# Kernel tuning notes

Hardware: AMD Instinct MI355X
Metric: run time of the kernel (lower is better)

## Reference

```python
import jax, jax.numpy as jnp
import numpy as np

T_NUM = 1024      # tracks
DET_NUM = 1024    # detections
DEG = 64          # candidate detections per track
E = T_NUM * DEG   # directed track->det edges (row<col half)
N = T_NUM + DET_NUM
D_IN = 512
D_EMB = 256
LAM = 5.0
SLACK = -0.2
SINKHORN_ITERS = 8


def setup_inputs() -> dict:
    key = jax.random.key(0)
    ks = jax.random.split(key, 20)
    x = jax.random.normal(ks[0], (N, D_IN), jnp.float32)
    coords = jax.random.uniform(ks[1], (N, 4), dtype=jnp.float32)
    r = jax.random.uniform(ks[2], (N, 4), dtype=jnp.float32)
    bx1 = r[:, 0] * 100.0; by1 = r[:, 1] * 100.0
    bw = r[:, 2] * 50.0 + 1.0; bh = r[:, 3] * 50.0 + 1.0
    coords_original = jnp.stack([bx1, by1, bx1 + bw, by1 + bh], axis=1)
    src_t = jnp.repeat(jnp.arange(T_NUM, dtype=jnp.int32), DEG)
    off = jnp.tile(jnp.arange(DEG, dtype=jnp.int32), T_NUM)
    dst_d = (src_t * 13 + off) % DET_NUM            # unique det per (track, slot)
    src = src_t
    dst = dst_d + T_NUM                              # detection node ids come after tracks
    edge_index = jnp.concatenate([jnp.stack([src, dst]), jnp.stack([dst, src])], axis=1)
    ground_truth = jax.random.bernoulli(ks[3], 0.1, (T_NUM * DET_NUM,)).astype(jnp.float32)

    def lin(k, i, o):
        return jax.random.normal(k, (i, o), jnp.float32) / np.sqrt(i).astype(np.float32)

    params = {
        'W_enc': lin(ks[4], D_IN, D_EMB), 'b_enc': jnp.zeros((D_EMB,), jnp.float32),
        'W1a': lin(ks[5], 2 * D_EMB, 64), 'b1a': jnp.zeros((64,), jnp.float32),
        'W2a': lin(ks[6], 64, 1), 'b2a': jnp.zeros((1,), jnp.float32),
        'W1g': lin(ks[7], 8, 16), 'b1g': jnp.zeros((16,), jnp.float32),
        'W2g': lin(ks[8], 16, 1), 'b2g': jnp.zeros((1,), jnp.float32),
        'W1f': lin(ks[9], 2, 8), 'b1f': jnp.zeros((8,), jnp.float32),
        'W2f': lin(ks[10], 8, 1), 'b2f': jnp.zeros((1,), jnp.float32),
        'Wn': lin(ks[11], D_EMB, D_EMB), 'Wm': lin(ks[12], D_EMB, D_EMB),
        'bo': jnp.zeros((D_EMB,), jnp.float32),
        'W1c': lin(ks[13], 2, 8), 'b1c': jnp.zeros((8,), jnp.float32),
        'W2c': lin(ks[14], 8, 1), 'b2c': jnp.zeros((1,), jnp.float32),
    }
    out = {'x': x, 'coords': coords, 'coords_original': coords_original,
           'ground_truth': ground_truth, 'edge_index': edge_index}
    out.update(params)
    return out


def _box_iou(a, b):
    # a, b: [E, 4] boxes (x1, y1, x2, y2)
    lt = jnp.maximum(a[:, :2], b[:, :2])
    rb = jnp.minimum(a[:, 2:], b[:, 2:])
    wh = jnp.clip(rb - lt, 0.0)
    inter = wh[:, 0] * wh[:, 1]
    area_a = (a[:, 2] - a[:, 0]) * (a[:, 3] - a[:, 1])
    area_b = (b[:, 2] - b[:, 0]) * (b[:, 3] - b[:, 1])
    return inter / (area_a + area_b - inter + 1e-9)


def _sinkhorn(M):
    def body(M, _):
        M = M / (jnp.sum(M, axis=1, keepdims=True) + 1e-9)
        M = M / (jnp.sum(M, axis=0, keepdims=True) + 1e-9)
        return M, None
    M, _ = jax.lax.scan(body, M, None, length=SINKHORN_ITERS)
    return M


def _forward(x, coords, coords_original,
             W_enc, b_enc, W1a, b1a, W2a, b2a, W1g, b1g, W2g, b2g,
             W1f, b1f, W2f, b2f, Wn, Wm, bo, W1c, b1c, W2c, b2c,
             edge_index):
    node = jax.nn.relu(x @ W_enc + b_enc)                      # [N, D_EMB]
    src, dst = edge_index[0], edge_index[1]                    # [2E]
    # batched per-edge appearance affinity (replaces python edge loop)
    pair = jnp.concatenate([node[src], node[dst]], axis=1)     # [2E, 2*D_EMB]
    a1 = jax.nn.relu(pair @ W1a + b1a) @ W2a + b2a             # [2E, 1]
    geo = jnp.concatenate([coords[src], coords[dst]], axis=1)  # [2E, 8]
    a2 = jax.nn.relu(geo @ W1g + b1g) @ W2g + b2g              # [2E, 1]
    e_in = jnp.concatenate([a1, a2], axis=1)                   # [2E, 2]
    edge_emb = jax.nn.relu(e_in @ W1f + b1f) @ W2f + b2f       # [2E, 1]
    # optim_net: one round of edge-weighted message passing
    msg = jax.ops.segment_sum(edge_emb * node[src], dst, num_segments=N)
    out = jax.nn.relu(node @ Wn + msg @ Wm + bo)               # [N, D_EMB]
    # forward (row < col) edges are the first E entries by construction
    sf, df = src[:E], dst[:E]
    oa, ob = out[sf], out[df]
    denom = jnp.maximum(jnp.linalg.norm(oa, axis=1) * jnp.linalg.norm(ob, axis=1), 1e-6)
    cosv = jnp.sum(oa * ob, axis=1) / denom                    # CosineSimilarity(dim=0) per edge
    iou = _box_iou(coords_original[sf], coords_original[df])   # [E]
    f_in = jnp.stack([cosv, iou], axis=1)                      # [E, 2]
    aff = (jax.nn.relu(f_in @ W1c + b1c) @ W2c + b2c)[:, 0]    # [E]
    # assignment matrix with slack row/col, scatter exp(aff*lam)
    slack_val = jnp.exp(jnp.float32(SLACK * LAM))
    M = jnp.full((T_NUM + 1, DET_NUM + 1), slack_val, jnp.float32)
    M = M.at[:T_NUM, :DET_NUM].set(0.0)
    M = M.at[sf, df - T_NUM].set(jnp.exp(aff * LAM))
    M = _sinkhorn(M)
    return M[:-1, :-1].reshape(-1)                             # [T_NUM*DET_NUM]


def reference(x, coords, coords_original, ground_truth, edge_index,
              W_enc, b_enc, W1a, b1a, W2a, b2a, W1g, b1g, W2g, b2g,
              W1f, b1f, W2f, b2f, Wn, Wm, bo, W1c, b1c, W2c, b2c):
    normalized_output = _forward(x, coords, coords_original,
                                 W_enc, b_enc, W1a, b1a, W2a, b2a,
                                 W1g, b1g, W2g, b2g, W1f, b1f, W2f, b2f,
                                 Wn, Wm, bo, W1c, b1c, W2c, b2c, edge_index)
    det_num = jnp.asarray(DET_NUM, jnp.int32)
    tracklet_num = jnp.asarray(T_NUM, jnp.int32)
    return (normalized_output, ground_truth, det_num, tracklet_num)
```

## Files before the change

kernel.cpp:

```cpp
#include <hip/hip_runtime.h>

#define T_NUM 1024
#define DET_NUM 1024
#define E_NUM 65536
#define TWO_E 131072
#define N_NODES 2048
#define D_IN 512
#define D_EMB 256

__device__ __forceinline__ unsigned bf16r(float x) {
  const unsigned u = __float_as_uint(x);
  return (u + 0x7fffu + ((u >> 16) & 1u)) >> 16;
}
__device__ __forceinline__ float bflo(unsigned p) { return __uint_as_float(p << 16); }
__device__ __forceinline__ float bfhi(unsigned p) { return __uint_as_float(p & 0xffff0000u); }

__global__ __launch_bounds__(512) void k_enc_pg(
    const float* __restrict__ x, const float* __restrict__ W,
    const float* __restrict__ b, const float* __restrict__ coords,
    const float* __restrict__ W1a, const float* __restrict__ W1g,
    float* __restrict__ node, float* __restrict__ P1, float* __restrict__ P2,
    float* __restrict__ G1, float* __restrict__ G2) {
  __shared__ __align__(16) float ns[8][D_EMB];
  __shared__ __align__(16) float ps[8][D_EMB];
  const int tid = threadIdx.x;
  const int j = tid & 255;
  const int h = __builtin_amdgcn_readfirstlane(tid >> 8);
  const int row0 = blockIdx.x * 8;
  float acc[8];
  const float bj = b[j];
#pragma unroll
  for (int r = 0; r < 8; r++) acc[r] = (h == 0) ? bj : 0.f;
  const float* xr = x + (size_t)row0 * D_IN + h * 256;
  const float* Wp = W + (size_t)h * 256 * D_EMB;
  for (int k = 0; k < 256; k += 4) {
    const float w0 = Wp[(k + 0) * D_EMB + j];
    const float w1 = Wp[(k + 1) * D_EMB + j];
    const float w2 = Wp[(k + 2) * D_EMB + j];
    const float w3 = Wp[(k + 3) * D_EMB + j];
#pragma unroll
    for (int r = 0; r < 8; r++) {
      const float4 xv = *reinterpret_cast<const float4*>(xr + (size_t)r * D_IN + k);
      acc[r] = fmaf(xv.x, w0, acc[r]);
      acc[r] = fmaf(xv.y, w1, acc[r]);
      acc[r] = fmaf(xv.z, w2, acc[r]);
      acc[r] = fmaf(xv.w, w3, acc[r]);
    }
  }
  if (h == 1) {
#pragma unroll
    for (int r = 0; r < 8; r++) ps[r][j] = acc[r];
  }
  __syncthreads();
  if (h == 0) {
#pragma unroll
    for (int r = 0; r < 8; r++) {
      const float v = fmaxf(acc[r] + ps[r][j], 0.f);
      node[(size_t)(row0 + r) * D_EMB + j] = v;
      ns[r][j] = v;
    }
  }
  __syncthreads();
  {
    const int r = tid >> 6, hh = tid & 63;
    float a1 = 0.f, a2 = 0.f;
    for (int k = 0; k < D_EMB; k += 4) {
      const float4 nv = *reinterpret_cast<const float4*>(&ns[r][k]);
      a1 = fmaf(nv.x, W1a[(k + 0) * 64 + hh], a1);
      a1 = fmaf(nv.y, W1a[(k + 1) * 64 + hh], a1);
      a1 = fmaf(nv.z, W1a[(k + 2) * 64 + hh], a1);
      a1 = fmaf(nv.w, W1a[(k + 3) * 64 + hh], a1);
      a2 = fmaf(nv.x, W1a[(D_EMB + k + 0) * 64 + hh], a2);
      a2 = fmaf(nv.y, W1a[(D_EMB + k + 1) * 64 + hh], a2);
      a2 = fmaf(nv.z, W1a[(D_EMB + k + 2) * 64 + hh], a2);
      a2 = fmaf(nv.w, W1a[(D_EMB + k + 3) * 64 + hh], a2);
    }
    P1[(size_t)(row0 + r) * 64 + hh] = a1;
    P2[(size_t)(row0 + r) * 64 + hh] = a2;
  }
  if (tid < 128) {
    const int r = tid >> 4, hh = tid & 15;
    const int n = row0 + r;
    float g1 = 0.f, g2 = 0.f;
#pragma unroll
    for (int k = 0; k < 4; k++) {
      const float c = coords[(size_t)n * 4 + k];
      g1 = fmaf(c, W1g[k * 16 + hh], g1);
      g2 = fmaf(c, W1g[(4 + k) * 16 + hh], g2);
    }
    G1[(size_t)n * 16 + hh] = g1;
    G2[(size_t)n * 16 + hh] = g2;
  }
}

__global__ __launch_bounds__(256) void k_edge(
    const float* __restrict__ P1, const float* __restrict__ P2,
    const float* __restrict__ G1, const float* __restrict__ G2,
    const float* __restrict__ b1a, const float* __restrict__ W2a, const float* __restrict__ b2a,
    const float* __restrict__ b1g, const float* __restrict__ W2g, const float* __restrict__ b2g,
    const float* __restrict__ W1f, const float* __restrict__ b1f,
    const float* __restrict__ W2f, const float* __restrict__ b2f,
    float* __restrict__ wE) {
  const int e = blockIdx.x * 256 + threadIdx.x;
  int s, dn;
  if (e < E_NUM) {
    const int t = e >> 6, o = e & 63;
    s = t; dn = T_NUM + ((13 * t + o) & 1023);
  } else {
    const int e2 = e - E_NUM;
    const int t = e2 >> 6, o = e2 & 63;
    s = T_NUM + ((13 * t + o) & 1023); dn = t;
  }
  const float4* p1 = (const float4*)(P1 + (size_t)s * 64);
  const float4* p2 = (const float4*)(P2 + (size_t)dn * 64);
  const float4* b1 = (const float4*)b1a;
  const float4* w2 = (const float4*)W2a;
  float a1 = b2a[0];
#pragma unroll
  for (int i = 0; i < 16; i++) {
    const float4 pa = p1[i], pb = p2[i], bb = b1[i], ww = w2[i];
    a1 += fmaxf(pa.x + pb.x + bb.x, 0.f) * ww.x + fmaxf(pa.y + pb.y + bb.y, 0.f) * ww.y +
          fmaxf(pa.z + pb.z + bb.z, 0.f) * ww.z + fmaxf(pa.w + pb.w + bb.w, 0.f) * ww.w;
  }
  const float4* g1 = (const float4*)(G1 + (size_t)s * 16);
  const float4* g2 = (const float4*)(G2 + (size_t)dn * 16);
  const float4* bg = (const float4*)b1g;
  const float4* wg = (const float4*)W2g;
  float a2 = b2g[0];
#pragma unroll
  for (int i = 0; i < 4; i++) {
    const float4 pa = g1[i], pb = g2[i], bb = bg[i], ww = wg[i];
    a2 += fmaxf(pa.x + pb.x + bb.x, 0.f) * ww.x + fmaxf(pa.y + pb.y + bb.y, 0.f) * ww.y +
          fmaxf(pa.z + pb.z + bb.z, 0.f) * ww.z + fmaxf(pa.w + pb.w + bb.w, 0.f) * ww.w;
  }
  float acc = b2f[0];
#pragma unroll
  for (int jj = 0; jj < 8; jj++) {
    const float h = fmaxf(a1 * W1f[jj] + a2 * W1f[8 + jj] + b1f[jj], 0.f);
    acc = fmaf(h, W2f[jj], acc);
  }
  wE[e] = acc;
}

__global__ __launch_bounds__(256) void k_msg_out(
    const float* __restrict__ wE, const float* __restrict__ node,
    const float* __restrict__ Wn, const float* __restrict__ Wm,
    const float* __restrict__ bo, float* __restrict__ outE, float* __restrict__ nrm) {
  __shared__ __align__(16) float ms[4][D_EMB];
  __shared__ float wsh[4][64];
  __shared__ int ssh[4][64];
  __shared__ float redn[4][4];
  const int j = threadIdx.x;
  const int lane = j & 63, wid = j >> 6;
  const int row0 = blockIdx.x * 4;
  {
    const int r = j >> 6, o = j & 63;
    const int n = row0 + r;
    int e, src;
    if (n < T_NUM) {
      e = E_NUM + n * 64 + o;
      src = T_NUM + ((13 * n + o) & 1023);
    } else {
      const int d = n - T_NUM;
      const int t = (709 * (d - o)) & 1023;
      e = t * 64 + o;
      src = t;
    }
    wsh[r][o] = wE[e];
    ssh[r][o] = src;
  }
  __syncthreads();
#pragma unroll 1
  for (int r = 0; r < 4; r++) {
    float acc = 0.f;
#pragma unroll 4
    for (int i = 0; i < 64; i++)
      acc = fmaf(wsh[r][i], node[(size_t)ssh[r][i] * D_EMB + j], acc);
    ms[r][j] = acc;
  }
  __syncthreads();
  float acc[4];
  const float bj = bo[j];
#pragma unroll
  for (int r = 0; r < 4; r++) acc[r] = bj;
  const float* nrow = node + (size_t)row0 * D_EMB;
  for (int k = 0; k < D_EMB; k += 4) {
    const float wn0 = Wn[(k + 0) * D_EMB + j], wm0 = Wm[(k + 0) * D_EMB + j];
    const float wn1 = Wn[(k + 1) * D_EMB + j], wm1 = Wm[(k + 1) * D_EMB + j];
    const float wn2 = Wn[(k + 2) * D_EMB + j], wm2 = Wm[(k + 2) * D_EMB + j];
    const float wn3 = Wn[(k + 3) * D_EMB + j], wm3 = Wm[(k + 3) * D_EMB + j];
#pragma unroll
    for (int r = 0; r < 4; r++) {
      const float4 nv = *reinterpret_cast<const float4*>(nrow + (size_t)r * D_EMB + k);
      const float4 mv = *reinterpret_cast<const float4*>(&ms[r][k]);
      acc[r] = fmaf(nv.x, wn0, acc[r]); acc[r] = fmaf(mv.x, wm0, acc[r]);
      acc[r] = fmaf(nv.y, wn1, acc[r]); acc[r] = fmaf(mv.y, wm1, acc[r]);
      acc[r] = fmaf(nv.z, wn2, acc[r]); acc[r] = fmaf(mv.z, wm2, acc[r]);
      acc[r] = fmaf(nv.w, wn3, acc[r]); acc[r] = fmaf(mv.w, wm3, acc[r]);
    }
  }
#pragma unroll
  for (int r = 0; r < 4; r++) {
    acc[r] = fmaxf(acc[r], 0.f);
    outE[(size_t)(row0 + r) * D_EMB + j] = acc[r];
  }
#pragma unroll
  for (int r = 0; r < 4; r++) {
    float sq = acc[r] * acc[r];
#pragma unroll
    for (int o = 32; o > 0; o >>= 1) sq += __shfl_down(sq, o, 64);
    if (lane == 0) redn[wid][r] = sq;
  }
  __syncthreads();
  if (j < 4)
    nrm[row0 + j] = sqrtf(redn[0][j] + redn[1][j] + redn[2][j] + redn[3][j]);
}

__global__ __launch_bounds__(256) void k_aff(
    const float* __restrict__ outE, const float* __restrict__ nrm,
    const float* __restrict__ cov,
    const float* __restrict__ W1c, const float* __restrict__ b1c,
    const float* __restrict__ W2c, const float* __restrict__ b2c,
    float* __restrict__ Kbp, unsigned short* __restrict__ KTg) {
  const int e = blockIdx.x * 256 + threadIdx.x;
  const int t = e >> 6, o = e & 63;
  const int s = t;
  const int d = (13 * t + o) & 1023;
  const int dn = T_NUM + d;
  const float4* oa = (const float4*)(outE + (size_t)s * D_EMB);
  const float4* ob = (const float4*)(outE + (size_t)dn * D_EMB);
  float dot = 0.f;
#pragma unroll 8
  for (int i = 0; i < 64; i++) {
    const float4 a = oa[i], bq = ob[i];
    dot += a.x * bq.x + a.y * bq.y + a.z * bq.z + a.w * bq.w;
  }
  const float cosv = dot / fmaxf(nrm[s] * nrm[dn], 1e-6f);
  const float4 A = ((const float4*)cov)[s];
  const float4 B = ((const float4*)cov)[dn];
  const float ltx = fmaxf(A.x, B.x), lty = fmaxf(A.y, B.y);
  const float rbx = fminf(A.z, B.z), rby = fminf(A.w, B.w);
  const float wx = fmaxf(rbx - ltx, 0.f), wy = fmaxf(rby - lty, 0.f);
  const float inter = wx * wy;
  const float areaA = (A.z - A.x) * (A.w - A.y);
  const float areaB = (B.z - B.x) * (B.w - B.y);
  const float iou = inter / (areaA + areaB - inter + 1e-9f);
  float aff = b2c[0];
#pragma unroll
  for (int jj = 0; jj < 8; jj++) {
    const float h = fmaxf(cosv * W1c[jj] + iou * W1c[8 + jj] + b1c[jj], 0.f);
    aff = fmaf(h, W2c[jj], aff);
  }
  const float Kv = __expf(aff * 5.0f);
  const int tp = (13 * s) & 1023;
  Kbp[tp * 68 + (tp & 3) + o] = Kv;
  if (o < 4) {
    const int pr = (o < (tp & 3)) ? o : o + 64;
    Kbp[tp * 68 + pr] = 0.f;
  }
  const int cbase = (((d & 1022) + 960) & 1023) & ~3;
  const int rho = (((d + 961) & 1023) - cbase) & 1023;
  KTg[d * 72 + rho + 63 - o] = (unsigned short)bf16r(Kv);
  if (o < 8) {
    const int slot = (o < rho) ? o : o + 64;
    KTg[d * 72 + slot] = 0;
  }
}

__global__ __launch_bounds__(512, 2) void k_sinkhorn(
    const float* __restrict__ Kbp, const unsigned short* __restrict__ KTg,
    float* __restrict__ ug, float* __restrict__ vg) {
  __shared__ __align__(16) float u_lds[1092];
  __shared__ __align__(16) float v_lds[1092];
  __shared__ float red_u[8];
  __shared__ float red_v[8];
  __shared__ __align__(16) uint4 ktlA[9][512];
  __shared__ __align__(16) uint4 ktlB[9][512];
  const int tid = threadIdx.x;
  const int lane = tid & 63, wid = tid >> 6;
  const int ra = 2 * tid, rb = 2 * tid + 1;
  const int qa = (ra & ~3) >> 2;
  const int cbase = ((ra + 960) & 1023) & ~3;
  const int qc = cbase >> 2;
  unsigned k0[34], k1[34];
  {
    const float4* s0p = (const float4*)(Kbp + (size_t)ra * 68);
    const float4* s1p = (const float4*)(Kbp + (size_t)rb * 68);
#pragma unroll
    for (int c = 0; c < 17; c++) {
      float4 f = s0p[c];
      k0[2 * c]     = bf16r(f.x) | (bf16r(f.y) << 16);
      k0[2 * c + 1] = bf16r(f.z) | (bf16r(f.w) << 16);
      f = s1p[c];
      k1[2 * c]     = bf16r(f.x) | (bf16r(f.y) << 16);
      k1[2 * c + 1] = bf16r(f.z) | (bf16r(f.w) << 16);
    }
  }
  {
    const uint4* g = (const uint4*)KTg;
#pragma unroll
    for (int q = 0; q < 9; q++) ktlA[q][tid] = g[tid * 18 + q];
#pragma unroll
    for (int q = 0; q < 9; q++) ktlB[q][tid] = g[tid * 18 + 9 + q];
  }
  float u0 = 1.f, u1 = 1.f, vc0 = 1.f, vc1 = 1.f, u_sl = 1.f, v_sl = 1.f;
  v_lds[tid] = 1.f; v_lds[tid + 512] = 1.f;
  if (tid < 68) v_lds[1024 + tid] = 1.f;
  if (tid < 8) red_v[tid] = 128.f;
  const float slack = 0.36787944117144233f;
  __syncthreads();
#pragma unroll 1
  for (int it = 0; it < 8; ++it) {
    const float4* vq = (const float4*)v_lds;
    float a00 = 0.f, a01 = 0.f, a10 = 0.f, a11 = 0.f;
#pragma unroll
    for (int c = 0; c < 17; c++) {
      const float4 v4 = vq[qa + c];
      unsigned p = k0[2 * c];
      a00 = fmaf(bflo(p), v4.x, a00); a00 = fmaf(bfhi(p), v4.y, a00);
      p = k0[2 * c + 1];
      a01 = fmaf(bflo(p), v4.z, a01); a01 = fmaf(bfhi(p), v4.w, a01);
      p = k1[2 * c];
      a10 = fmaf(bflo(p), v4.x, a10); a10 = fmaf(bfhi(p), v4.y, a10);
      p = k1[2 * c + 1];
      a11 = fmaf(bflo(p), v4.z, a11); a11 = fmaf(bfhi(p), v4.w, a11);
    }
    const float sumv = red_v[0] + red_v[1] + red_v[2] + red_v[3] +
                       red_v[4] + red_v[5] + red_v[6] + red_v[7];
    const float s0 = a00 + a01 + slack * v_sl;
    const float s1 = a10 + a11 + slack * v_sl;
    u0 = u0 / (u0 * s0 + 1e-9f);
    u1 = u1 / (u1 * s1 + 1e-9f);
    u_sl = u_sl / (u_sl * slack * (sumv + v_sl) + 1e-9f);
    u_lds[ra] = u0; u_lds[rb] = u1;
    if (tid < 34) { u_lds[1024 + ra] = u0; u_lds[1024 + rb] = u1; }
    float usum = u0 + u1;
#pragma unroll
    for (int o = 32; o > 0; o >>= 1) usum += __shfl_down(usum, o, 64);
    if (lane == 0) red_u[wid] = usum;
    __syncthreads();
    const float4* uq = (const float4*)u_lds;
    float t0 = 0.f, t1 = 0.f;
#pragma unroll 3
    for (int q = 0; q < 9; q++) {
      const uint4 A = ktlA[q][tid];
      const uint4 B = ktlB[q][tid];
      const float4 ua = uq[qc + 2 * q];
      const float4 ub = uq[qc + 2 * q + 1];
      t0 = fmaf(bflo(A.x), ua.x, t0); t0 = fmaf(bfhi(A.x), ua.y, t0);
      t0 = fmaf(bflo(A.y), ua.z, t0); t0 = fmaf(bfhi(A.y), ua.w, t0);
      t0 = fmaf(bflo(A.z), ub.x, t0); t0 = fmaf(bfhi(A.z), ub.y, t0);
      t0 = fmaf(bflo(A.w), ub.z, t0); t0 = fmaf(bfhi(A.w), ub.w, t0);
      t1 = fmaf(bflo(B.x), ua.x, t1); t1 = fmaf(bfhi(B.x), ua.y, t1);
      t1 = fmaf(bflo(B.y), ua.z, t1); t1 = fmaf(bfhi(B.y), ua.w, t1);
      t1 = fmaf(bflo(B.z), ub.x, t1); t1 = fmaf(bfhi(B.z), ub.y, t1);
      t1 = fmaf(bflo(B.w), ub.z, t1); t1 = fmaf(bfhi(B.w), ub.w, t1);
    }
    const float sumu = red_u[0] + red_u[1] + red_u[2] + red_u[3] +
                       red_u[4] + red_u[5] + red_u[6] + red_u[7];
    t0 += slack * u_sl;
    t1 += slack * u_sl;
    vc0 = vc0 / (vc0 * t0 + 1e-9f);
    vc1 = vc1 / (vc1 * t1 + 1e-9f);
    v_sl = v_sl / (v_sl * slack * (sumu + u_sl) + 1e-9f);
    v_lds[ra] = vc0; v_lds[rb] = vc1;
    if (tid < 34) { v_lds[1024 + ra] = vc0; v_lds[1024 + rb] = vc1; }
    float vsum = vc0 + vc1;
#pragma unroll
    for (int o = 32; o > 0; o >>= 1) vsum += __shfl_down(vsum, o, 64);
    if (lane == 0) red_v[wid] = vsum;
    __syncthreads();
  }
  ((float2*)ug)[tid] = make_float2(u0, u1);
  ((float2*)vg)[tid] = make_float2(vc0, vc1);
}

__global__ __launch_bounds__(256) void k_final(
    const float* __restrict__ Kbp, const float* __restrict__ ug,
    const float* __restrict__ vg, const float* __restrict__ gt,
    float* __restrict__ out) {
  const int t = blockIdx.x;
  const int tp = (13 * t) & 1023;
  const float u = ug[tp];
  const float* krow = Kbp + (size_t)tp * 68 + (tp & 3);
  const int d0 = threadIdx.x * 4;
  const float4 v4 = ((const float4*)vg)[threadIdx.x];
  float4 o4;
  const int m0 = (d0 - tp) & 1023;
  const int m1 = (d0 + 1 - tp) & 1023;
  const int m2 = (d0 + 2 - tp) & 1023;
  const int m3 = (d0 + 3 - tp) & 1023;
  o4.x = (m0 < 64) ? u * krow[m0] * v4.x : 0.f;
  o4.y = (m1 < 64) ? u * krow[m1] * v4.y : 0.f;
  o4.z = (m2 < 64) ? u * krow[m2] * v4.z : 0.f;
  o4.w = (m3 < 64) ? u * krow[m3] * v4.w : 0.f;
  ((float4*)out)[(size_t)t * 256 + threadIdx.x] = o4;
  const float4 g4 = ((const float4*)gt)[(size_t)t * 256 + threadIdx.x];
  ((float4*)out)[(size_t)(T_NUM + t) * 256 + threadIdx.x] = g4;
  if (t == 0 && threadIdx.x == 0) {
    out[(size_t)2 * T_NUM * DET_NUM] = 1024.0f;
    out[(size_t)2 * T_NUM * DET_NUM + 1] = 1024.0f;
  }
}

extern "C" void kernel_launch(void* const* d_in, const int* in_sizes, int n_in,
                              void* d_out, int out_size, void* d_ws, size_t ws_size,
                              hipStream_t stream) {
  const float* x      = (const float*)d_in[0];
  const float* coords = (const float*)d_in[1];
  const float* cov    = (const float*)d_in[2];
  const float* gt     = (const float*)d_in[3];
  const float* W_enc  = (const float*)d_in[5];
  const float* b_enc  = (const float*)d_in[6];
  const float* W1a    = (const float*)d_in[7];
  const float* b1a    = (const float*)d_in[8];
  const float* W2a    = (const float*)d_in[9];
  const float* b2a    = (const float*)d_in[10];
  const float* W1g    = (const float*)d_in[11];
  const float* b1g    = (const float*)d_in[12];
  const float* W2g    = (const float*)d_in[13];
  const float* b2g    = (const float*)d_in[14];
  const float* W1f    = (const float*)d_in[15];
  const float* b1f    = (const float*)d_in[16];
  const float* W2f    = (const float*)d_in[17];
  const float* b2f    = (const float*)d_in[18];
  const float* Wn     = (const float*)d_in[19];
  const float* Wm     = (const float*)d_in[20];
  const float* bo     = (const float*)d_in[21];
  const float* W1c    = (const float*)d_in[22];
  const float* b1c    = (const float*)d_in[23];
  const float* W2c    = (const float*)d_in[24];
  const float* b2c    = (const float*)d_in[25];

  char* ws = (char*)d_ws;
  size_t off = 0;
  auto alloc = [&](size_t bytes) {
    char* p = ws + off;
    off = (off + bytes + 255) & ~(size_t)255;
    return p;
  };
  float* node  = (float*)alloc((size_t)N_NODES * D_EMB * 4);
  float* P1    = (float*)alloc((size_t)N_NODES * 64 * 4);
  float* P2    = (float*)alloc((size_t)N_NODES * 64 * 4);
  float* G1    = (float*)alloc((size_t)N_NODES * 16 * 4);
  float* G2    = (float*)alloc((size_t)N_NODES * 16 * 4);
  float* wE    = (float*)alloc((size_t)TWO_E * 4);
  float* outE  = (float*)alloc((size_t)N_NODES * D_EMB * 4);
  float* nrm   = (float*)alloc((size_t)N_NODES * 4);
  float* Kbp   = (float*)alloc((size_t)1024 * 68 * 4);
  unsigned short* KTg = (unsigned short*)alloc((size_t)1024 * 72 * 2);
  float* ug    = (float*)alloc(1024 * 4);
  float* vg    = (float*)alloc(1024 * 4);
  float* out   = (float*)d_out;

  k_enc_pg<<<N_NODES / 8, 512, 0, stream>>>(x, W_enc, b_enc, coords, W1a, W1g,
                                            node, P1, P2, G1, G2);
  k_edge<<<TWO_E / 256, 256, 0, stream>>>(P1, P2, G1, G2, b1a, W2a, b2a,
                                          b1g, W2g, b2g, W1f, b1f, W2f, b2f, wE);
  k_msg_out<<<N_NODES / 4, 256, 0, stream>>>(wE, node, Wn, Wm, bo, outE, nrm);
  k_aff<<<E_NUM / 256, 256, 0, stream>>>(outE, nrm, cov, W1c, b1c, W2c, b2c,
                                         Kbp, KTg);
  k_sinkhorn<<<1, 512, 0, stream>>>(Kbp, KTg, ug, vg);
  k_final<<<T_NUM, 256, 0, stream>>>(Kbp, ug, vg, gt, out);
}
```

Measured before the change: 221.9 us.

## Fuse edge-weight MLP into message kernel and split affinity dot across waves

Removes the separate k_edge kernel and the wE buffer. Each message block now computes its own incoming edge weights inline from P1/P2/G1/G2, which saves one launch and a global round trip. The affinity kernel now uses one block per track: the track's embedding is staged in shared memory and each of the 256-element dot products is split across four waves, with a shared-memory reduction afterwards. In exchange, the epilogue of the affinity kernel runs on only 64 of 256 threads and there are extra barriers.

Measured after the change: 221.2 us. Within noise of the previous version (-0.3%).

```diff
diff --git a/kernel.cpp b/kernel.cpp
--- a/kernel.cpp
+++ b/kernel.cpp
@@ -93,57 +93,14 @@
   }
 }
 
-__global__ __launch_bounds__(256) void k_edge(
+__global__ __launch_bounds__(256) void k_msg_out(
+    const float* __restrict__ node,
     const float* __restrict__ P1, const float* __restrict__ P2,
     const float* __restrict__ G1, const float* __restrict__ G2,
     const float* __restrict__ b1a, const float* __restrict__ W2a, const float* __restrict__ b2a,
     const float* __restrict__ b1g, const float* __restrict__ W2g, const float* __restrict__ b2g,
     const float* __restrict__ W1f, const float* __restrict__ b1f,
     const float* __restrict__ W2f, const float* __restrict__ b2f,
-    float* __restrict__ wE) {
-  const int e = blockIdx.x * 256 + threadIdx.x;
-  int s, dn;
-  if (e < E_NUM) {
-    const int t = e >> 6, o = e & 63;
-    s = t; dn = T_NUM + ((13 * t + o) & 1023);
-  } else {
-    const int e2 = e - E_NUM;
-    const int t = e2 >> 6, o = e2 & 63;
-    s = T_NUM + ((13 * t + o) & 1023); dn = t;
-  }
-  const float4* p1 = (const float4*)(P1 + (size_t)s * 64);
-  const float4* p2 = (const float4*)(P2 + (size_t)dn * 64);
-  const float4* b1 = (const float4*)b1a;
-  const float4* w2 = (const float4*)W2a;
-  float a1 = b2a[0];
-#pragma unroll
-  for (int i = 0; i < 16; i++) {
-    const float4 pa = p1[i], pb = p2[i], bb = b1[i], ww = w2[i];
-    a1 += fmaxf(pa.x + pb.x + bb.x, 0.f) * ww.x + fmaxf(pa.y + pb.y + bb.y, 0.f) * ww.y +
-          fmaxf(pa.z + pb.z + bb.z, 0.f) * ww.z + fmaxf(pa.w + pb.w + bb.w, 0.f) * ww.w;
-  }
-  const float4* g1 = (const float4*)(G1 + (size_t)s * 16);
-  const float4* g2 = (const float4*)(G2 + (size_t)dn * 16);
-  const float4* bg = (const float4*)b1g;
-  const float4* wg = (const float4*)W2g;
-  float a2 = b2g[0];
-#pragma unroll
-  for (int i = 0; i < 4; i++) {
-    const float4 pa = g1[i], pb = g2[i], bb = bg[i], ww = wg[i];
-    a2 += fmaxf(pa.x + pb.x + bb.x, 0.f) * ww.x + fmaxf(pa.y + pb.y + bb.y, 0.f) * ww.y +
-          fmaxf(pa.z + pb.z + bb.z, 0.f) * ww.z + fmaxf(pa.w + pb.w + bb.w, 0.f) * ww.w;
-  }
-  float acc = b2f[0];
-#pragma unroll
-  for (int jj = 0; jj < 8; jj++) {
-    const float h = fmaxf(a1 * W1f[jj] + a2 * W1f[8 + jj] + b1f[jj], 0.f);
-    acc = fmaf(h, W2f[jj], acc);
-  }
-  wE[e] = acc;
-}
-
-__global__ __launch_bounds__(256) void k_msg_out(
-    const float* __restrict__ wE, const float* __restrict__ node,
     const float* __restrict__ Wn, const float* __restrict__ Wm,
     const float* __restrict__ bo, float* __restrict__ outE, float* __restrict__ nrm) {
   __shared__ __align__(16) float ms[4][D_EMB];
@@ -156,17 +113,42 @@
   {
     const int r = j >> 6, o = j & 63;
     const int n = row0 + r;
-    int e, src;
+    int src;
     if (n < T_NUM) {
-      e = E_NUM + n * 64 + o;
       src = T_NUM + ((13 * n + o) & 1023);
     } else {
       const int d = n - T_NUM;
-      const int t = (709 * (d - o)) & 1023;
-      e = t * 64 + o;
-      src = t;
-    }
-    wsh[r][o] = wE[e];
+      src = (709 * (d - o)) & 1023;
+    }
+    const float4* p1 = (const float4*)(P1 + (size_t)src * 64);
+    const float4* p2 = (const float4*)(P2 + (size_t)n * 64);
+    const float4* b1 = (const float4*)b1a;
+    const float4* w2 = (const float4*)W2a;
+    float a1 = b2a[0];
+#pragma unroll
+    for (int i = 0; i < 16; i++) {
+      const float4 pa = p1[i], pb = p2[i], bb = b1[i], ww = w2[i];
+      a1 += fmaxf(pa.x + pb.x + bb.x, 0.f) * ww.x + fmaxf(pa.y + pb.y + bb.y, 0.f) * ww.y +
+            fmaxf(pa.z + pb.z + bb.z, 0.f) * ww.z + fmaxf(pa.w + pb.w + bb.w, 0.f) * ww.w;
+    }
+    const float4* g1 = (const float4*)(G1 + (size_t)src * 16);
+    const float4* g2 = (const float4*)(G2 + (size_t)n * 16);
+    const float4* bg = (const float4*)b1g;
+    const float4* wg = (const float4*)W2g;
+    float a2 = b2g[0];
+#pragma unroll
+    for (int i = 0; i < 4; i++) {
+      const float4 pa = g1[i], pb = g2[i], bb = bg[i], ww = wg[i];
+      a2 += fmaxf(pa.x + pb.x + bb.x, 0.f) * ww.x + fmaxf(pa.y + pb.y + bb.y, 0.f) * ww.y +
+            fmaxf(pa.z + pb.z + bb.z, 0.f) * ww.z + fmaxf(pa.w + pb.w + bb.w, 0.f) * ww.w;
+    }
+    float acc = b2f[0];
+#pragma unroll
+    for (int jj = 0; jj < 8; jj++) {
+      const float h = fmaxf(a1 * W1f[jj] + a2 * W1f[8 + jj] + b1f[jj], 0.f);
+      acc = fmaf(h, W2f[jj], acc);
+    }
+    wsh[r][o] = acc;
     ssh[r][o] = src;
   }
   __syncthreads();
@@ -222,48 +204,60 @@
     const float* __restrict__ W1c, const float* __restrict__ b1c,
     const float* __restrict__ W2c, const float* __restrict__ b2c,
     float* __restrict__ Kbp, unsigned short* __restrict__ KTg) {
-  const int e = blockIdx.x * 256 + threadIdx.x;
-  const int t = e >> 6, o = e & 63;
+  __shared__ __align__(16) float4 oas[64];
+  __shared__ float psum[4][64];
+  const int t = blockIdx.x;
+  const int tid = threadIdx.x;
+  const int o = tid & 63, c = tid >> 6;
   const int s = t;
+  if (tid < 64) oas[tid] = ((const float4*)(outE + (size_t)s * D_EMB))[tid];
+  __syncthreads();
   const int d = (13 * t + o) & 1023;
   const int dn = T_NUM + d;
-  const float4* oa = (const float4*)(outE + (size_t)s * D_EMB);
-  const float4* ob = (const float4*)(outE + (size_t)dn * D_EMB);
-  float dot = 0.f;
-#pragma unroll 8
-  for (int i = 0; i < 64; i++) {
-    const float4 a = oa[i], bq = ob[i];
-    dot += a.x * bq.x + a.y * bq.y + a.z * bq.z + a.w * bq.w;
-  }
-  const float cosv = dot / fmaxf(nrm[s] * nrm[dn], 1e-6f);
-  const float4 A = ((const float4*)cov)[s];
-  const float4 B = ((const float4*)cov)[dn];
-  const float ltx = fmaxf(A.x, B.x), lty = fmaxf(A.y, B.y);
-  const float rbx = fminf(A.z, B.z), rby = fminf(A.w, B.w);
-  const float wx = fmaxf(rbx - ltx, 0.f), wy = fmaxf(rby - lty, 0.f);
-  const float inter = wx * wy;
-  const float areaA = (A.z - A.x) * (A.w - A.y);
-  const float areaB = (B.z - B.x) * (B.w - B.y);
-  const float iou = inter / (areaA + areaB - inter + 1e-9f);
-  float aff = b2c[0];
-#pragma unroll
-  for (int jj = 0; jj < 8; jj++) {
-    const float h = fmaxf(cosv * W1c[jj] + iou * W1c[8 + jj] + b1c[jj], 0.f);
-    aff = fmaf(h, W2c[jj], aff);
-  }
-  const float Kv = __expf(aff * 5.0f);
-  const int tp = (13 * s) & 1023;
-  Kbp[tp * 68 + (tp & 3) + o] = Kv;
-  if (o < 4) {
-    const int pr = (o < (tp & 3)) ? o : o + 64;
-    Kbp[tp * 68 + pr] = 0.f;
-  }
-  const int cbase = (((d & 1022) + 960) & 1023) & ~3;
-  const int rho = (((d + 961) & 1023) - cbase) & 1023;
-  KTg[d * 72 + rho + 63 - o] = (unsigned short)bf16r(Kv);
-  if (o < 8) {
-    const int slot = (o < rho) ? o : o + 64;
-    KTg[d * 72 + slot] = 0;
+  {
+    const float4* ob = (const float4*)(outE + (size_t)dn * D_EMB) + c * 16;
+    const float4* oa = oas + c * 16;
+    float dot = 0.f;
+#pragma unroll
+    for (int i = 0; i < 16; i++) {
+      const float4 a = oa[i], bq = ob[i];
+      dot += a.x * bq.x + a.y * bq.y + a.z * bq.z + a.w * bq.w;
+    }
+    psum[c][o] = dot;
+  }
+  __syncthreads();
+  if (tid < 64) {
+    const float dot = psum[0][o] + psum[1][o] + psum[2][o] + psum[3][o];
+    const float cosv = dot / fmaxf(nrm[s] * nrm[dn], 1e-6f);
+    const float4 A = ((const float4*)cov)[s];
+    const float4 B = ((const float4*)cov)[dn];
+    const float ltx = fmaxf(A.x, B.x), lty = fmaxf(A.y, B.y);
+    const float rbx = fminf(A.z, B.z), rby = fminf(A.w, B.w);
+    const float wx = fmaxf(rbx - ltx, 0.f), wy = fmaxf(rby - lty, 0.f);
+    const float inter = wx * wy;
+    const float areaA = (A.z - A.x) * (A.w - A.y);
+    const float areaB = (B.z - B.x) * (B.w - B.y);
+    const float iou = inter / (areaA + areaB - inter + 1e-9f);
+    float aff = b2c[0];
+#pragma unroll
+    for (int jj = 0; jj < 8; jj++) {
+      const float h = fmaxf(cosv * W1c[jj] + iou * W1c[8 + jj] + b1c[jj], 0.f);
+      aff = fmaf(h, W2c[jj], aff);
+    }
+    const float Kv = __expf(aff * 5.0f);
+    const int tp = (13 * s) & 1023;
+    Kbp[tp * 68 + (tp & 3) + o] = Kv;
+    if (o < 4) {
+      const int pr = (o < (tp & 3)) ? o : o + 64;
+      Kbp[tp * 68 + pr] = 0.f;
+    }
+    const int cbase = (((d & 1022) + 960) & 1023) & ~3;
+    const int rho = (((d + 961) & 1023) - cbase) & 1023;
+    KTg[d * 72 + rho + 63 - o] = (unsigned short)bf16r(Kv);
+    if (o < 8) {
+      const int slot = (o < rho) ? o : o + 64;
+      KTg[d * 72 + slot] = 0;
+    }
   }
 }
 
@@ -444,7 +438,6 @@
   float* P2    = (float*)alloc((size_t)N_NODES * 64 * 4);
   float* G1    = (float*)alloc((size_t)N_NODES * 16 * 4);
   float* G2    = (float*)alloc((size_t)N_NODES * 16 * 4);
-  float* wE    = (float*)alloc((size_t)TWO_E * 4);
   float* outE  = (float*)alloc((size_t)N_NODES * D_EMB * 4);
   float* nrm   = (float*)alloc((size_t)N_NODES * 4);
   float* Kbp   = (float*)alloc((size_t)1024 * 68 * 4);
@@ -455,11 +448,12 @@
 
   k_enc_pg<<<N_NODES / 8, 512, 0, stream>>>(x, W_enc, b_enc, coords, W1a, W1g,
                                             node, P1, P2, G1, G2);
-  k_edge<<<TWO_E / 256, 256, 0, stream>>>(P1, P2, G1, G2, b1a, W2a, b2a,
-                                          b1g, W2g, b2g, W1f, b1f, W2f, b2f, wE);
-  k_msg_out<<<N_NODES / 4, 256, 0, stream>>>(wE, node, Wn, Wm, bo, outE, nrm);
-  k_aff<<<E_NUM / 256, 256, 0, stream>>>(outE, nrm, cov, W1c, b1c, W2c, b2c,
-                                         Kbp, KTg);
+  k_msg_out<<<N_NODES / 4, 256, 0, stream>>>(node, P1, P2, G1, G2,
+                                             b1a, W2a, b2a, b1g, W2g, b2g,
+                                             W1f, b1f, W2f, b2f,
+                                             Wn, Wm, bo, outE, nrm);
+  k_aff<<<T_NUM, 256, 0, stream>>>(outE, nrm, cov, W1c, b1c, W2c, b2c,
+                                   Kbp, KTg);
   k_sinkhorn<<<1, 512, 0, stream>>>(Kbp, KTg, ug, vg);
   k_final<<<T_NUM, 256, 0, stream>>>(Kbp, ug, vg, gt, out);
 }
```
